# Kernel optimization log

Hardware: AMD Instinct MI355X
Metric: run time of the kernel (lower is better)

Reference implementation:

```python
import jax, jax.numpy as jnp
import numpy as np

THRESHOLD = 0.5
NEG_POS_RATIO = 3
ALPHA = 1.0
BETA = 1.0
IGNORE_INDEX = 255

B, P, C, O = 16, 16384, 21, 16
H = W = 256


def cxcy_to_xy(c):
    return jnp.concatenate([c[..., :2] - c[..., 2:] / 2, c[..., :2] + c[..., 2:] / 2], axis=-1)


def xy_to_cxcy(xy):
    return jnp.concatenate([(xy[..., :2] + xy[..., 2:]) / 2, xy[..., 2:] - xy[..., :2]], axis=-1)


def cxcy_to_gcxgcy(cxcy, priors_cxcy):
    return jnp.concatenate([
        (cxcy[..., :2] - priors_cxcy[..., :2]) / (priors_cxcy[..., 2:] / 10.0),
        jnp.log(cxcy[..., 2:] / priors_cxcy[..., 2:]) * 5.0,
    ], axis=-1)


def jaccard(set1, set2):
    # set1 [O,4] xy, set2 [P,4] xy -> IoU [O,P]
    lo = jnp.maximum(set1[:, None, :2], set2[None, :, :2])
    hi = jnp.minimum(set1[:, None, 2:], set2[None, :, 2:])
    wh = jnp.clip(hi - lo, 0.0)
    inter = wh[..., 0] * wh[..., 1]
    a1 = (set1[:, 2] - set1[:, 0]) * (set1[:, 3] - set1[:, 1])
    a2 = (set2[:, 2] - set2[:, 0]) * (set2[:, 3] - set2[:, 1])
    return inter / (a1[:, None] + a2[None, :] - inter)


def setup_inputs() -> dict:
    key = jax.random.key(0)
    ks = jax.random.split(key, 8)
    predicted_locs = jax.random.normal(ks[0], (B, P, 4), dtype=jnp.float32)
    predicted_scores = jax.random.normal(ks[1], (B, P, C), dtype=jnp.float32)
    predicted_masks = jax.random.normal(ks[2], (B, C, H, W), dtype=jnp.float32)
    x1y1 = jax.random.uniform(ks[3], (B, O, 2), dtype=jnp.float32) * 0.8
    wh = jax.random.uniform(ks[4], (B, O, 2), dtype=jnp.float32) * 0.19 + 0.01
    boxes = jnp.concatenate([x1y1, x1y1 + wh], axis=-1)  # valid xy boxes
    pc = jax.random.uniform(ks[5], (P, 2), dtype=jnp.float32) * 0.9 + 0.05
    pwh = jax.random.uniform(ks[6], (P, 2), dtype=jnp.float32) * 0.28 + 0.02
    priors_cxcy = jnp.concatenate([pc, pwh], axis=-1)
    labels = jax.random.randint(ks[7], (B, O), 1, C)  # object labels, never background
    masks = jax.random.randint(jax.random.fold_in(key, 99), (B, 1, H, W), 0, C)
    return {
        'predicted_locs': predicted_locs,
        'predicted_scores': predicted_scores,
        'predicted_masks': predicted_masks,
        'boxes': boxes,
        'priors_cxcy': priors_cxcy,
        'labels': labels,
        'masks': masks,
    }


def _assign(bx, lb, priors_cxcy, priors_xy):
    # bx [O,4] xy, lb [O] int -> true_locs [P,4], true_classes [P]
    ov = jaccard(bx, priors_xy)  # [O,P]
    overlap_for_each_prior = ov.max(axis=0)       # [P]
    object_for_each_prior = ov.argmax(axis=0)     # [P]
    prior_for_each_object = ov.argmax(axis=1)     # [O]
    # guarantee every object is matched to its best prior
    object_for_each_prior = object_for_each_prior.at[prior_for_each_object].set(jnp.arange(O))
    overlap_for_each_prior = overlap_for_each_prior.at[prior_for_each_object].set(1.0)
    label_for_each_prior = lb[object_for_each_prior]
    label_for_each_prior = jnp.where(overlap_for_each_prior < THRESHOLD, 0, label_for_each_prior)
    true_locs = cxcy_to_gcxgcy(xy_to_cxcy(bx[object_for_each_prior]), priors_cxcy)
    return true_locs, label_for_each_prior


def reference(predicted_locs, predicted_scores, predicted_masks, boxes, priors_cxcy, labels, masks):
    priors_xy = cxcy_to_xy(priors_cxcy)
    true_locs, true_classes = jax.vmap(_assign, in_axes=(0, 0, None, None))(
        boxes, labels, priors_cxcy, priors_xy)  # [B,P,4], [B,P]

    pos = true_classes != 0                      # [B,P]
    pos_f = pos.astype(predicted_locs.dtype)
    n_pos = pos.sum(axis=1)                      # [B]

    # localization: L1Loss (mean over positive prior elements)
    diff = jnp.abs(predicted_locs - true_locs)
    loc_loss = (diff * pos_f[..., None]).sum() / jnp.maximum(pos_f.sum() * 4.0, 1.0)

    # confidence: CE per prior + hard negative mining
    logp = jax.nn.log_softmax(predicted_scores, axis=-1)            # [B,P,C]
    ce = -jnp.take_along_axis(logp, true_classes[..., None], axis=-1)[..., 0]  # [B,P]
    ce_pos_sum = (ce * pos_f).sum()
    ce_neg = jnp.where(pos, 0.0, ce)
    ce_neg_sorted = -jnp.sort(-ce_neg, axis=1)                      # descending
    ranks = jnp.arange(P)[None, :]
    hard = (ranks < (NEG_POS_RATIO * n_pos)[:, None]).astype(ce.dtype)
    ce_hardneg_sum = (ce_neg_sorted * hard).sum()
    conf_loss = (ce_hardneg_sum + ce_pos_sum) / n_pos.sum().astype(ce.dtype)

    # mask loss: cross_entropy2d, sum reduction then / (H*W) / B
    tgt = masks[:, 0]                                                # [B,H,W]
    valid = (tgt != IGNORE_INDEX)
    t = jnp.where(valid, tgt, 0)
    logp_m = jax.nn.log_softmax(predicted_masks, axis=1)             # [B,C,H,W]
    ce_m = -jnp.take_along_axis(logp_m, t[:, None], axis=1)[:, 0]    # [B,H,W]
    mask_loss = (ce_m * valid.astype(ce_m.dtype)).sum() / (H * W) / B

    return conf_loss + ALPHA * loc_loss + BETA * mask_loss
```

## Files before the change

kernel.cpp:

```cpp
#include <hip/hip_runtime.h>
#include <cstdint>
#include <cstddef>

#define Bn 16
#define Pn 16384
#define Cn 21
#define On 16
#define HWn 65536
#define THRESH 0.5f

typedef float f4v __attribute__((ext_vector_type(4)));


__device__ __forceinline__ float waveReduceSum(float v) {
  for (int off = 32; off > 0; off >>= 1) v += __shfl_down(v, off, 64);
  return v;
}
__device__ __forceinline__ int waveReduceSumI(int v) {
  for (int off = 32; off > 0; off >>= 1) v += __shfl_down(v, off, 64);
  return v;
}

__global__ __launch_bounds__(256) void k_phase1(
    const float* __restrict__ boxes, const float* __restrict__ priors,
    unsigned long long* __restrict__ partials, int* __restrict__ done_cnt) {
  const int lane = threadIdx.x & 63, wave = threadIdx.x >> 6;
  __shared__ float4 sbox[On];
  __shared__ float sarea[On];
  __shared__ unsigned long long skey[On];
  if (blockIdx.x == 0 && threadIdx.x == 0) *done_cnt = 0;

  const int b = blockIdx.x >> 6;
  const int p0 = (blockIdx.x & 63) << 8;
  const int p = p0 + threadIdx.x;
  if (threadIdx.x < On) {
    float4 bx = ((const float4*)boxes)[b * On + threadIdx.x];
    sbox[threadIdx.x] = bx;
    sarea[threadIdx.x] = (bx.z - bx.x) * (bx.w - bx.y);
    skey[threadIdx.x] = 0ULL;
  }
  __syncthreads();
  float4 pr = ((const float4*)priors)[p];
  const float px1 = pr.x - 0.5f * pr.z, py1 = pr.y - 0.5f * pr.w;
  const float px2 = pr.x + 0.5f * pr.z, py2 = pr.y + 0.5f * pr.w;
  const float parea = pr.z * pr.w;
#pragma unroll
  for (int o = 0; o < On; ++o) {
    float4 bx = sbox[o];
    float ix = fmaxf(fminf(px2, bx.z) - fmaxf(px1, bx.x), 0.f);
    float iy = fmaxf(fminf(py2, bx.w) - fmaxf(py1, bx.y), 0.f);
    float inter = ix * iy;
    float iou = inter / (sarea[o] + parea - inter);
    float m = iou;
#pragma unroll
    for (int off = 32; off > 0; off >>= 1) m = fmaxf(m, __shfl_xor(m, off, 64));
    unsigned long long tie = __ballot(iou == m);
    if (lane == 0) {
      int lmin = __ffsll(tie) - 1;
      unsigned minp = (unsigned)(p0 + (wave << 6) + lmin);
      unsigned long long key = ((unsigned long long)__float_as_uint(m) << 32) |
                               (unsigned long long)(0xFFFFFFFFu - minp);
      atomicMax(&skey[o], key);
    }
  }
  __syncthreads();
  if (threadIdx.x < On)
    partials[(size_t)blockIdx.x * On + threadIdx.x] = skey[threadIdx.x];
}

__global__ __launch_bounds__(256, 2) void k_assign(
    const float* __restrict__ plocs, const float* __restrict__ pscores,
    const float* __restrict__ boxes, const float* __restrict__ priors,
    const int* __restrict__ labels, const unsigned long long* __restrict__ partials,
    float* __restrict__ ce_neg, float* __restrict__ apart_loc,
    float* __restrict__ apart_ce, int* __restrict__ apart_npos) {
  __shared__ float ssc[256 * Cn];
  __shared__ float4 sbox[On];
  __shared__ float sarea[On];
  __shared__ int slab[On];
  __shared__ int spfo[On];
  __shared__ unsigned long long skey[On];
  __shared__ float sr1[4], sr2[4];
  __shared__ int sri[4];
  const int lane = threadIdx.x & 63, wave = threadIdx.x >> 6;
  const int b = blockIdx.x >> 6;
  const int p0 = (blockIdx.x & 63) << 8;
  const int p = p0 + threadIdx.x;
  {
    const float4* src = (const float4*)(pscores + ((size_t)b * Pn + p0) * Cn);
    float4* dst = (float4*)ssc;
#pragma unroll
    for (int i = threadIdx.x; i < (256 * Cn) / 4; i += 256) dst[i] = src[i];
  }
  if (threadIdx.x < On) {
    float4 bx = ((const float4*)boxes)[b * On + threadIdx.x];
    sbox[threadIdx.x] = bx;
    sarea[threadIdx.x] = (bx.z - bx.x) * (bx.w - bx.y);
    slab[threadIdx.x] = labels[b * On + threadIdx.x];
    skey[threadIdx.x] = 0ULL;
  }
  __syncthreads();
  {
    const int o = threadIdx.x & 15, j = threadIdx.x >> 4;
    const unsigned long long* pp = partials + ((size_t)b * 64) * On;
    unsigned long long k = 0ULL;
#pragma unroll
    for (int t = 0; t < 4; ++t) {
      unsigned long long v = pp[(size_t)(j * 4 + t) * On + o];
      k = v > k ? v : k;
    }
    atomicMax(&skey[o], k);
  }
  __syncthreads();
  if (threadIdx.x < On)
    spfo[threadIdx.x] = (int)(0xFFFFFFFFu - (unsigned)(skey[threadIdx.x] & 0xFFFFFFFFULL));
  __syncthreads();

  float4 pr = ((const float4*)priors)[p];
  const float px1 = pr.x - 0.5f * pr.z, py1 = pr.y - 0.5f * pr.w;
  const float px2 = pr.x + 0.5f * pr.z, py2 = pr.y + 0.5f * pr.w;
  const float parea = pr.z * pr.w;
  float best = -1.f;
  int bobj = 0;
#pragma unroll
  for (int o = 0; o < On; ++o) {
    float4 bx = sbox[o];
    float ix = fmaxf(fminf(px2, bx.z) - fmaxf(px1, bx.x), 0.f);
    float iy = fmaxf(fminf(py2, bx.w) - fmaxf(py1, bx.y), 0.f);
    float inter = ix * iy;
    float iou = inter / (sarea[o] + parea - inter);
    if (iou > best) { best = iou; bobj = o; }
  }
#pragma unroll
  for (int o = 0; o < On; ++o) {
    if (spfo[o] == p) { bobj = o; best = 1.0f; }
  }
  const int lbl = (best < THRESH) ? 0 : slab[bobj];
  const bool pos = (lbl != 0);
  float locp = 0.f;
  if (pos) {
    float4 bx = sbox[bobj];
    float cx = 0.5f * (bx.x + bx.z), cy = 0.5f * (bx.y + bx.w);
    float w = bx.z - bx.x, h = bx.w - bx.y;
    float g0 = (cx - pr.x) / (pr.z * 0.1f);
    float g1 = (cy - pr.y) / (pr.w * 0.1f);
    float g2 = logf(w / pr.z) * 5.f;
    float g3 = logf(h / pr.w) * 5.f;
    float4 pl = ((const float4*)plocs)[b * Pn + p];
    locp = fabsf(pl.x - g0) + fabsf(pl.y - g1) + fabsf(pl.z - g2) + fabsf(pl.w - g3);
  }
  const float* my = ssc + threadIdx.x * Cn;
  float s = 0.f, xt = 0.f;
#pragma unroll
  for (int c = 0; c < Cn; ++c) {
    float v = my[c];
    s += __expf(v);
    if (c == lbl) xt = v;
  }
  float ce = __logf(s) - xt;
  ce_neg[b * Pn + p] = pos ? 0.f : ce;
  float cep = pos ? ce : 0.f;

  float r1 = waveReduceSum(locp);
  float r2 = waveReduceSum(cep);
  int ri = waveReduceSumI(pos ? 1 : 0);
  if (lane == 0) { sr1[wave] = r1; sr2[wave] = r2; sri[wave] = ri; }
  __syncthreads();
  if (threadIdx.x == 0) {
    apart_loc[blockIdx.x] = sr1[0] + sr1[1] + sr1[2] + sr1[3];
    apart_ce[blockIdx.x] = sr2[0] + sr2[1] + sr2[2] + sr2[3];
    apart_npos[blockIdx.x] = sri[0] + sri[1] + sri[2] + sri[3];
  }
}

__global__ __launch_bounds__(512, 4) void k_hnmask_final(
    const float* __restrict__ ce_neg, const int* __restrict__ apart_npos,
    const float* __restrict__ apart_loc, const float* __restrict__ apart_ce,
    const float* __restrict__ pm, const int* __restrict__ msk,
    float* __restrict__ bres, float* __restrict__ mpart,
    int* __restrict__ done_cnt, float* __restrict__ out) {
  const int tid = threadIdx.x;
  const int lane = tid & 63, wave = tid >> 6;
  __shared__ int scnt[8];
  __shared__ float ssum[8];
  __shared__ float sce[8], smk[8], shn[8];
  __shared__ int sK;
  __shared__ int stick;

  if (blockIdx.x < Bn) {
    const int b = blockIdx.x;
    unsigned rv[32];
#pragma unroll
    for (int i = 0; i < 32; ++i)
      rv[i] = __float_as_uint(ce_neg[b * Pn + i * 512 + tid]);
    if (wave == 0) {
      int v = apart_npos[b * 64 + lane];
      v = waveReduceSumI(v);
      if (lane == 0) sK = v;
    }
    __syncthreads();
    int K = 3 * sK;
    if (K > Pn) K = Pn;
    unsigned lo = 0u, hi = 0x7F800000u;
    while (lo < hi) {
      unsigned mid = lo + ((hi - lo) >> 1);
      int c = 0;
#pragma unroll
      for (int i = 0; i < 32; ++i) c += (rv[i] > mid) ? 1 : 0;
      c = waveReduceSumI(c);
      if (lane == 0) scnt[wave] = c;
      __syncthreads();
      int total = 0;
#pragma unroll
      for (int w = 0; w < 8; ++w) total += scnt[w];
      if (total < K) hi = mid; else lo = mid + 1;
      __syncthreads();
    }
    const float fv = __uint_as_float(lo);
    float s = 0.f;
    int c = 0;
#pragma unroll
    for (int i = 0; i < 32; ++i) {
      if (rv[i] > lo) { s += __uint_as_float(rv[i]); c++; }
    }
    s = waveReduceSum(s);
    c = waveReduceSumI(c);
    if (lane == 0) { ssum[wave] = s; scnt[wave] = c; }
    __syncthreads();
    if (tid == 0) {
      float tots = 0.f;
      int totc = 0;
#pragma unroll
      for (int w = 0; w < 8; ++w) { tots += ssum[w]; totc += scnt[w]; }
      bres[b] = tots + (float)(K - totc) * fv;
    }
  } else {
    const int t = blockIdx.x - Bn;
    float contrib = 0.f;
#pragma unroll
    for (int q = 0; q < 2; ++q) {
      const int idx4 = t * 1024 + q * 512 + tid;
      const int b = idx4 >> 14;
      const int pix = (idx4 & 16383) << 2;
      int4 t4 = ((const int4*)msk)[idx4];
      const float* base = pm + (size_t)b * ((size_t)Cn * HWn) + pix;
#define M_LD(i)                                                              \
  f4v v##i;                                                                  \
  {                                                                          \
    const float* a##i = base + (size_t)(i) * HWn;                            \
    asm volatile("global_load_dwordx4 %0, %1, off"                           \
                 : "=&v"(v##i) : "v"(a##i));                                 \
  }
      M_LD(0) M_LD(1) M_LD(2) M_LD(3) M_LD(4) M_LD(5) M_LD(6) M_LD(7)
      M_LD(8) M_LD(9) M_LD(10) M_LD(11) M_LD(12) M_LD(13) M_LD(14) M_LD(15)
      M_LD(16) M_LD(17) M_LD(18) M_LD(19) M_LD(20)
#undef M_LD
      asm volatile("s_waitcnt vmcnt(0)" ::: "memory");
      __builtin_amdgcn_sched_barrier(0);
      const bool w0 = (t4.x != 255), w1 = (t4.y != 255), w2 = (t4.z != 255),
                 w3 = (t4.w != 255);
      const int c0 = w0 ? t4.x : 0, c1 = w1 ? t4.y : 0, c2 = w2 ? t4.z : 0,
                c3 = w3 ? t4.w : 0;
      float s0 = 0.f, s1 = 0.f, s2 = 0.f, s3 = 0.f;
      float x0 = 0.f, x1 = 0.f, x2 = 0.f, x3 = 0.f;
#define M_ACC(i)                                                             \
  {                                                                          \
    s0 += __expf(v##i.x); s1 += __expf(v##i.y);                              \
    s2 += __expf(v##i.z); s3 += __expf(v##i.w);                              \
    if (c0 == i) x0 = v##i.x; if (c1 == i) x1 = v##i.y;                      \
    if (c2 == i) x2 = v##i.z; if (c3 == i) x3 = v##i.w;                      \
  }
      M_ACC(0) M_ACC(1) M_ACC(2) M_ACC(3) M_ACC(4) M_ACC(5) M_ACC(6) M_ACC(7)
      M_ACC(8) M_ACC(9) M_ACC(10) M_ACC(11) M_ACC(12) M_ACC(13) M_ACC(14)
      M_ACC(15) M_ACC(16) M_ACC(17) M_ACC(18) M_ACC(19) M_ACC(20)
#undef M_ACC
      contrib += (w0 ? (__logf(s0) - x0) : 0.f) +
                 (w1 ? (__logf(s1) - x1) : 0.f) +
                 (w2 ? (__logf(s2) - x2) : 0.f) +
                 (w3 ? (__logf(s3) - x3) : 0.f);
    }
    float r = waveReduceSum(contrib);
    if (lane == 0) ssum[wave] = r;
    __syncthreads();
    if (tid == 0) {
      float acc = 0.f;
#pragma unroll
      for (int w = 0; w < 8; ++w) acc += ssum[w];
      mpart[t] = acc;
    }
  }

  __syncthreads();
  if (tid == 0) {
    __threadfence();
    stick = atomicAdd(done_cnt, 1);
  }
  __syncthreads();
  if (stick != Bn + 256 - 1) return;
  __threadfence();
  float l_loc = apart_loc[tid] + apart_loc[tid + 512];
  float l_ce = apart_ce[tid] + apart_ce[tid + 512];
  int l_np = apart_npos[tid] + apart_npos[tid + 512];
  float l_msk = (tid < 256) ? atomicAdd(&mpart[tid], 0.f) : 0.f;
  float l_hn = (tid < Bn) ? atomicAdd(&bres[tid], 0.f) : 0.f;
  l_loc = waveReduceSum(l_loc);
  l_ce = waveReduceSum(l_ce);
  l_msk = waveReduceSum(l_msk);
  l_hn = waveReduceSum(l_hn);
  int l_npw = waveReduceSumI(l_np);
  if (lane == 0) {
    ssum[wave] = l_loc;
    sce[wave] = l_ce;
    smk[wave] = l_msk;
    shn[wave] = l_hn;
    scnt[wave] = l_npw;
  }
  __syncthreads();
  if (tid == 0) {
    float a0 = 0.f, a1 = 0.f, a2 = 0.f, a3 = 0.f;
    int np_i = 0;
#pragma unroll
    for (int w = 0; w < 8; ++w) {
      a0 += ssum[w]; a1 += sce[w]; a3 += smk[w]; a2 += shn[w];
      np_i += scnt[w];
    }
    float np = (float)np_i;
    float conf = (a2 + a1) / np;
    float loc = a0 / fmaxf(np * 4.f, 1.f);
    float maskl = a3 / (float)HWn / (float)Bn;
    out[0] = conf + loc + maskl;
  }
}

extern "C" void kernel_launch(void* const* d_in, const int* in_sizes, int n_in,
                              void* d_out, int out_size, void* d_ws, size_t ws_size,
                              hipStream_t stream) {
  const float* plocs   = (const float*)d_in[0];
  const float* pscores = (const float*)d_in[1];
  const float* pmasks  = (const float*)d_in[2];
  const float* boxes   = (const float*)d_in[3];
  const float* priors  = (const float*)d_in[4];
  const int*   labels  = (const int*)d_in[5];
  const int*   masks   = (const int*)d_in[6];

  char* ws = (char*)d_ws;
  float* mpart = (float*)ws;
  unsigned long long* partials = (unsigned long long*)(ws + 4096);
  float* ce_neg = (float*)(ws + 135168);
  float* apart_loc = (float*)(ws + 1183744);
  float* apart_ce = (float*)(ws + 1187840);
  int* apart_npos = (int*)(ws + 1191936);
  float* bres = (float*)(ws + 1196032);
  int* done_cnt = (int*)(ws + 1196160);

  k_phase1<<<1024, 256, 0, stream>>>(boxes, priors, partials, done_cnt);
  k_assign<<<1024, 256, 0, stream>>>(plocs, pscores, boxes, priors, labels,
                                     partials, ce_neg, apart_loc, apart_ce,
                                     apart_npos);
  k_hnmask_final<<<Bn + 256, 512, 0, stream>>>(ce_neg, apart_npos, apart_loc,
                                               apart_ce, pmasks, masks, bres,
                                               mpart, done_cnt, (float*)d_out);
}
```

Measured before the change: 190.2 us.

## Spread mask cross-entropy slices across all three kernels to overlap with assignment

The 256 mask-loss slices, which all ran in the final kernel, are now split: 86 run alongside phase-1 IoU matching, 85 alongside assignment/CE, and 85 alongside hard-negative mining. Phase-1 and assign blocks are widened to 512 threads, each handling two prior tiles. The aim is to fill the GPU with memory-bound mask work while the lighter stages run, and to shorten the tail of the last kernel. In exchange the block roles become heterogeneous, and assign blocks need twice the shared memory, which may cut occupancy.

```diff
diff --git a/kernel.cpp b/kernel.cpp
--- a/kernel.cpp
+++ b/kernel.cpp
@@ -21,26 +21,95 @@
   return v;
 }
 
-__global__ __launch_bounds__(256) void k_phase1(
+__device__ __forceinline__ void maskSlice(const float* __restrict__ pm,
+                                          const int* __restrict__ msk,
+                                          float* __restrict__ mpart,
+                                          int m, int tid, float* ssum8) {
+  const int lane = tid & 63, wv = tid >> 6;
+  float contrib = 0.f;
+#pragma unroll
+  for (int q = 0; q < 2; ++q) {
+    const int idx4 = m * 1024 + q * 512 + tid;
+    const int b = idx4 >> 14;
+    const int pix = (idx4 & 16383) << 2;
+    int4 t4 = ((const int4*)msk)[idx4];
+    const float* base = pm + (size_t)b * ((size_t)Cn * HWn) + pix;
+#define M_LD(i)                                                              \
+  f4v v##i;                                                                  \
+  {                                                                          \
+    const float* a##i = base + (size_t)(i) * HWn;                            \
+    asm volatile("global_load_dwordx4 %0, %1, off"                           \
+                 : "=&v"(v##i) : "v"(a##i));                                 \
+  }
+    M_LD(0) M_LD(1) M_LD(2) M_LD(3) M_LD(4) M_LD(5) M_LD(6) M_LD(7)
+    M_LD(8) M_LD(9) M_LD(10) M_LD(11) M_LD(12) M_LD(13) M_LD(14) M_LD(15)
+    M_LD(16) M_LD(17) M_LD(18) M_LD(19) M_LD(20)
+#undef M_LD
+    asm volatile("s_waitcnt vmcnt(0)" ::: "memory");
+    __builtin_amdgcn_sched_barrier(0);
+    const bool w0 = (t4.x != 255), w1 = (t4.y != 255), w2 = (t4.z != 255),
+               w3 = (t4.w != 255);
+    const int c0 = w0 ? t4.x : 0, c1 = w1 ? t4.y : 0, c2 = w2 ? t4.z : 0,
+              c3 = w3 ? t4.w : 0;
+    float s0 = 0.f, s1 = 0.f, s2 = 0.f, s3 = 0.f;
+    float x0 = 0.f, x1 = 0.f, x2 = 0.f, x3 = 0.f;
+#define M_ACC(i)                                                             \
+  {                                                                          \
+    s0 += __expf(v##i.x); s1 += __expf(v##i.y);                              \
+    s2 += __expf(v##i.z); s3 += __expf(v##i.w);                              \
+    if (c0 == i) x0 = v##i.x; if (c1 == i) x1 = v##i.y;                      \
+    if (c2 == i) x2 = v##i.z; if (c3 == i) x3 = v##i.w;                      \
+  }
+    M_ACC(0) M_ACC(1) M_ACC(2) M_ACC(3) M_ACC(4) M_ACC(5) M_ACC(6) M_ACC(7)
+    M_ACC(8) M_ACC(9) M_ACC(10) M_ACC(11) M_ACC(12) M_ACC(13) M_ACC(14)
+    M_ACC(15) M_ACC(16) M_ACC(17) M_ACC(18) M_ACC(19) M_ACC(20)
+#undef M_ACC
+    contrib += (w0 ? (__logf(s0) - x0) : 0.f) +
+               (w1 ? (__logf(s1) - x1) : 0.f) +
+               (w2 ? (__logf(s2) - x2) : 0.f) +
+               (w3 ? (__logf(s3) - x3) : 0.f);
+  }
+  float r = waveReduceSum(contrib);
+  if (lane == 0) ssum8[wv] = r;
+  __syncthreads();
+  if (tid == 0) {
+    float acc = 0.f;
+#pragma unroll
+    for (int w = 0; w < 8; ++w) acc += ssum8[w];
+    mpart[m] = acc;
+  }
+}
+
+__global__ __launch_bounds__(512, 4) void k1_p1mask(
     const float* __restrict__ boxes, const float* __restrict__ priors,
-    unsigned long long* __restrict__ partials, int* __restrict__ done_cnt) {
-  const int lane = threadIdx.x & 63, wave = threadIdx.x >> 6;
+    const float* __restrict__ pm, const int* __restrict__ msk,
+    unsigned long long* __restrict__ partials, float* __restrict__ mpart,
+    int* __restrict__ done_cnt) {
   __shared__ float4 sbox[On];
   __shared__ float sarea[On];
-  __shared__ unsigned long long skey[On];
-  if (blockIdx.x == 0 && threadIdx.x == 0) *done_cnt = 0;
-
-  const int b = blockIdx.x >> 6;
-  const int p0 = (blockIdx.x & 63) << 8;
-  const int p = p0 + threadIdx.x;
-  if (threadIdx.x < On) {
-    float4 bx = ((const float4*)boxes)[b * On + threadIdx.x];
-    sbox[threadIdx.x] = bx;
-    sarea[threadIdx.x] = (bx.z - bx.x) * (bx.w - bx.y);
-    skey[threadIdx.x] = 0ULL;
-  }
-  __syncthreads();
-  float4 pr = ((const float4*)priors)[p];
+  __shared__ unsigned long long skey2[2][On];
+  __shared__ float ssum8[8];
+  const int tid = threadIdx.x;
+  if (blockIdx.x == 0 && tid == 0) *done_cnt = 0;
+
+  if (blockIdx.x < 86) {
+    maskSlice(pm, msk, mpart, blockIdx.x, tid, ssum8);
+    return;
+  }
+  const int T = blockIdx.x - 86;
+  const int h = tid >> 8, t256 = tid & 255;
+  const int lane = tid & 63;
+  const int task = 2 * T + h;
+  const int b = task >> 6;
+  const int p0 = (task & 63) << 8;
+  if (tid < On) {
+    float4 bx = ((const float4*)boxes)[b * On + tid];
+    sbox[tid] = bx;
+    sarea[tid] = (bx.z - bx.x) * (bx.w - bx.y);
+  }
+  if (t256 < On) skey2[h][t256] = 0ULL;
+  __syncthreads();
+  float4 pr = ((const float4*)priors)[p0 + t256];
   const float px1 = pr.x - 0.5f * pr.z, py1 = pr.y - 0.5f * pr.w;
   const float px2 = pr.x + 0.5f * pr.z, py2 = pr.y + 0.5f * pr.w;
   const float parea = pr.z * pr.w;
@@ -57,51 +126,61 @@
     unsigned long long tie = __ballot(iou == m);
     if (lane == 0) {
       int lmin = __ffsll(tie) - 1;
-      unsigned minp = (unsigned)(p0 + (wave << 6) + lmin);
+      unsigned minp = (unsigned)(p0 + ((t256 >> 6) << 6) + lmin);
       unsigned long long key = ((unsigned long long)__float_as_uint(m) << 32) |
                                (unsigned long long)(0xFFFFFFFFu - minp);
-      atomicMax(&skey[o], key);
-    }
-  }
-  __syncthreads();
-  if (threadIdx.x < On)
-    partials[(size_t)blockIdx.x * On + threadIdx.x] = skey[threadIdx.x];
-}
-
-__global__ __launch_bounds__(256, 2) void k_assign(
+      atomicMax(&skey2[h][o], key);
+    }
+  }
+  __syncthreads();
+  if (t256 < On)
+    partials[(size_t)task * On + t256] = skey2[h][t256];
+}
+
+__global__ __launch_bounds__(512, 4) void k2_assignmask(
     const float* __restrict__ plocs, const float* __restrict__ pscores,
     const float* __restrict__ boxes, const float* __restrict__ priors,
     const int* __restrict__ labels, const unsigned long long* __restrict__ partials,
+    const float* __restrict__ pm, const int* __restrict__ msk,
     float* __restrict__ ce_neg, float* __restrict__ apart_loc,
-    float* __restrict__ apart_ce, int* __restrict__ apart_npos) {
-  __shared__ float ssc[256 * Cn];
+    float* __restrict__ apart_ce, int* __restrict__ apart_npos,
+    float* __restrict__ mpart) {
+  __shared__ float ssc[2 * 256 * Cn];
   __shared__ float4 sbox[On];
   __shared__ float sarea[On];
   __shared__ int slab[On];
   __shared__ int spfo[On];
   __shared__ unsigned long long skey[On];
-  __shared__ float sr1[4], sr2[4];
-  __shared__ int sri[4];
-  const int lane = threadIdx.x & 63, wave = threadIdx.x >> 6;
-  const int b = blockIdx.x >> 6;
-  const int p0 = (blockIdx.x & 63) << 8;
-  const int p = p0 + threadIdx.x;
+  __shared__ float sr1[8], sr2[8];
+  __shared__ int sri[8];
+  const int tid = threadIdx.x;
+  if (blockIdx.x < 85) {
+    maskSlice(pm, msk, mpart, 86 + blockIdx.x, tid, sr1);
+    return;
+  }
+  const int T = blockIdx.x - 85;
+  const int h = tid >> 8, t256 = tid & 255;
+  const int lane = tid & 63, wv = tid >> 6;
+  const int task = 2 * T + h;
+  const int b = task >> 6;
+  const int p0 = (task & 63) << 8;
+  const int p = p0 + t256;
   {
     const float4* src = (const float4*)(pscores + ((size_t)b * Pn + p0) * Cn);
-    float4* dst = (float4*)ssc;
-#pragma unroll
-    for (int i = threadIdx.x; i < (256 * Cn) / 4; i += 256) dst[i] = src[i];
-  }
-  if (threadIdx.x < On) {
-    float4 bx = ((const float4*)boxes)[b * On + threadIdx.x];
-    sbox[threadIdx.x] = bx;
-    sarea[threadIdx.x] = (bx.z - bx.x) * (bx.w - bx.y);
-    slab[threadIdx.x] = labels[b * On + threadIdx.x];
-    skey[threadIdx.x] = 0ULL;
-  }
-  __syncthreads();
-  {
-    const int o = threadIdx.x & 15, j = threadIdx.x >> 4;
+    float4* dst = (float4*)(ssc + h * (256 * Cn));
+#pragma unroll
+    for (int i = t256; i < (256 * Cn) / 4; i += 256) dst[i] = src[i];
+  }
+  if (tid < On) {
+    float4 bx = ((const float4*)boxes)[b * On + tid];
+    sbox[tid] = bx;
+    sarea[tid] = (bx.z - bx.x) * (bx.w - bx.y);
+    slab[tid] = labels[b * On + tid];
+    skey[tid] = 0ULL;
+  }
+  __syncthreads();
+  if (tid < 256) {
+    const int o = tid & 15, j = tid >> 4;
     const unsigned long long* pp = partials + ((size_t)b * 64) * On;
     unsigned long long k = 0ULL;
 #pragma unroll
@@ -112,8 +191,8 @@
     atomicMax(&skey[o], k);
   }
   __syncthreads();
-  if (threadIdx.x < On)
-    spfo[threadIdx.x] = (int)(0xFFFFFFFFu - (unsigned)(skey[threadIdx.x] & 0xFFFFFFFFULL));
+  if (tid < On)
+    spfo[tid] = (int)(0xFFFFFFFFu - (unsigned)(skey[tid] & 0xFFFFFFFFULL));
   __syncthreads();
 
   float4 pr = ((const float4*)priors)[p];
@@ -141,15 +220,16 @@
   if (pos) {
     float4 bx = sbox[bobj];
     float cx = 0.5f * (bx.x + bx.z), cy = 0.5f * (bx.y + bx.w);
-    float w = bx.z - bx.x, h = bx.w - bx.y;
+    float w = bx.z - bx.x, hh = bx.w - bx.y;
     float g0 = (cx - pr.x) / (pr.z * 0.1f);
     float g1 = (cy - pr.y) / (pr.w * 0.1f);
     float g2 = logf(w / pr.z) * 5.f;
-    float g3 = logf(h / pr.w) * 5.f;
+    float g3 = logf(hh / pr.w) * 5.f;
     float4 pl = ((const float4*)plocs)[b * Pn + p];
-    locp = fabsf(pl.x - g0) + fabsf(pl.y - g1) + fabsf(pl.z - g2) + fabsf(pl.w - g3);
-  }
-  const float* my = ssc + threadIdx.x * Cn;
+    locp = fabsf(pl.x - g0) + fabsf(pl.y - g1) + fabsf(pl.z - g2) +
+           fabsf(pl.w - g3);
+  }
+  const float* my = ssc + h * (256 * Cn) + t256 * Cn;
   float s = 0.f, xt = 0.f;
 #pragma unroll
   for (int c = 0; c < Cn; ++c) {
@@ -164,23 +244,28 @@
   float r1 = waveReduceSum(locp);
   float r2 = waveReduceSum(cep);
   int ri = waveReduceSumI(pos ? 1 : 0);
-  if (lane == 0) { sr1[wave] = r1; sr2[wave] = r2; sri[wave] = ri; }
-  __syncthreads();
-  if (threadIdx.x == 0) {
-    apart_loc[blockIdx.x] = sr1[0] + sr1[1] + sr1[2] + sr1[3];
-    apart_ce[blockIdx.x] = sr2[0] + sr2[1] + sr2[2] + sr2[3];
-    apart_npos[blockIdx.x] = sri[0] + sri[1] + sri[2] + sri[3];
-  }
-}
-
-__global__ __launch_bounds__(512, 4) void k_hnmask_final(
+  if (lane == 0) { sr1[wv] = r1; sr2[wv] = r2; sri[wv] = ri; }
+  __syncthreads();
+  if (tid == 0) {
+    apart_loc[task] = sr1[0] + sr1[1] + sr1[2] + sr1[3];
+    apart_ce[task] = sr2[0] + sr2[1] + sr2[2] + sr2[3];
+    apart_npos[task] = sri[0] + sri[1] + sri[2] + sri[3];
+  }
+  if (tid == 256) {
+    apart_loc[task] = sr1[4] + sr1[5] + sr1[6] + sr1[7];
+    apart_ce[task] = sr2[4] + sr2[5] + sr2[6] + sr2[7];
+    apart_npos[task] = sri[4] + sri[5] + sri[6] + sri[7];
+  }
+}
+
+__global__ __launch_bounds__(512, 4) void k3_hnmask_final(
     const float* __restrict__ ce_neg, const int* __restrict__ apart_npos,
     const float* __restrict__ apart_loc, const float* __restrict__ apart_ce,
     const float* __restrict__ pm, const int* __restrict__ msk,
     float* __restrict__ bres, float* __restrict__ mpart,
     int* __restrict__ done_cnt, float* __restrict__ out) {
   const int tid = threadIdx.x;
-  const int lane = tid & 63, wave = tid >> 6;
+  const int lane = tid & 63, wv = tid >> 6;
   __shared__ int scnt[8];
   __shared__ float ssum[8];
   __shared__ float sce[8], smk[8], shn[8];
@@ -193,7 +278,7 @@
 #pragma unroll
     for (int i = 0; i < 32; ++i)
       rv[i] = __float_as_uint(ce_neg[b * Pn + i * 512 + tid]);
-    if (wave == 0) {
+    if (wv == 0) {
       int v = apart_npos[b * 64 + lane];
       v = waveReduceSumI(v);
       if (lane == 0) sK = v;
@@ -208,7 +293,7 @@
 #pragma unroll
       for (int i = 0; i < 32; ++i) c += (rv[i] > mid) ? 1 : 0;
       c = waveReduceSumI(c);
-      if (lane == 0) scnt[wave] = c;
+      if (lane == 0) scnt[wv] = c;
       __syncthreads();
       int total = 0;
 #pragma unroll
@@ -225,7 +310,7 @@
     }
     s = waveReduceSum(s);
     c = waveReduceSumI(c);
-    if (lane == 0) { ssum[wave] = s; scnt[wave] = c; }
+    if (lane == 0) { ssum[wv] = s; scnt[wv] = c; }
     __syncthreads();
     if (tid == 0) {
       float tots = 0.f;
@@ -235,59 +320,7 @@
       bres[b] = tots + (float)(K - totc) * fv;
     }
   } else {
-    const int t = blockIdx.x - Bn;
-    float contrib = 0.f;
-#pragma unroll
-    for (int q = 0; q < 2; ++q) {
-      const int idx4 = t * 1024 + q * 512 + tid;
-      const int b = idx4 >> 14;
-      const int pix = (idx4 & 16383) << 2;
-      int4 t4 = ((const int4*)msk)[idx4];
-      const float* base = pm + (size_t)b * ((size_t)Cn * HWn) + pix;
-#define M_LD(i)                                                              \
-  f4v v##i;                                                                  \
-  {                                                                          \
-    const float* a##i = base + (size_t)(i) * HWn;                            \
-    asm volatile("global_load_dwordx4 %0, %1, off"                           \
-                 : "=&v"(v##i) : "v"(a##i));                                 \
-  }
-      M_LD(0) M_LD(1) M_LD(2) M_LD(3) M_LD(4) M_LD(5) M_LD(6) M_LD(7)
-      M_LD(8) M_LD(9) M_LD(10) M_LD(11) M_LD(12) M_LD(13) M_LD(14) M_LD(15)
-      M_LD(16) M_LD(17) M_LD(18) M_LD(19) M_LD(20)
-#undef M_LD
-      asm volatile("s_waitcnt vmcnt(0)" ::: "memory");
-      __builtin_amdgcn_sched_barrier(0);
-      const bool w0 = (t4.x != 255), w1 = (t4.y != 255), w2 = (t4.z != 255),
-                 w3 = (t4.w != 255);
-      const int c0 = w0 ? t4.x : 0, c1 = w1 ? t4.y : 0, c2 = w2 ? t4.z : 0,
-                c3 = w3 ? t4.w : 0;
-      float s0 = 0.f, s1 = 0.f, s2 = 0.f, s3 = 0.f;
-      float x0 = 0.f, x1 = 0.f, x2 = 0.f, x3 = 0.f;
-#define M_ACC(i)                                                             \
-  {                                                                          \
-    s0 += __expf(v##i.x); s1 += __expf(v##i.y);                              \
-    s2 += __expf(v##i.z); s3 += __expf(v##i.w);                              \
-    if (c0 == i) x0 = v##i.x; if (c1 == i) x1 = v##i.y;                      \
-    if (c2 == i) x2 = v##i.z; if (c3 == i) x3 = v##i.w;                      \
-  }
-      M_ACC(0) M_ACC(1) M_ACC(2) M_ACC(3) M_ACC(4) M_ACC(5) M_ACC(6) M_ACC(7)
-      M_ACC(8) M_ACC(9) M_ACC(10) M_ACC(11) M_ACC(12) M_ACC(13) M_ACC(14)
-      M_ACC(15) M_ACC(16) M_ACC(17) M_ACC(18) M_ACC(19) M_ACC(20)
-#undef M_ACC
-      contrib += (w0 ? (__logf(s0) - x0) : 0.f) +
-                 (w1 ? (__logf(s1) - x1) : 0.f) +
-                 (w2 ? (__logf(s2) - x2) : 0.f) +
-                 (w3 ? (__logf(s3) - x3) : 0.f);
-    }
-    float r = waveReduceSum(contrib);
-    if (lane == 0) ssum[wave] = r;
-    __syncthreads();
-    if (tid == 0) {
-      float acc = 0.f;
-#pragma unroll
-      for (int w = 0; w < 8; ++w) acc += ssum[w];
-      mpart[t] = acc;
-    }
+    maskSlice(pm, msk, mpart, 171 + (blockIdx.x - Bn), tid, ssum);
   }
 
   __syncthreads();
@@ -296,7 +329,7 @@
     stick = atomicAdd(done_cnt, 1);
   }
   __syncthreads();
-  if (stick != Bn + 256 - 1) return;
+  if (stick != Bn + 85 - 1) return;
   __threadfence();
   float l_loc = apart_loc[tid] + apart_loc[tid + 512];
   float l_ce = apart_ce[tid] + apart_ce[tid + 512];
@@ -309,11 +342,11 @@
   l_hn = waveReduceSum(l_hn);
   int l_npw = waveReduceSumI(l_np);
   if (lane == 0) {
-    ssum[wave] = l_loc;
-    sce[wave] = l_ce;
-    smk[wave] = l_msk;
-    shn[wave] = l_hn;
-    scnt[wave] = l_npw;
+    ssum[wv] = l_loc;
+    sce[wv] = l_ce;
+    smk[wv] = l_msk;
+    shn[wv] = l_hn;
+    scnt[wv] = l_npw;
   }
   __syncthreads();
   if (tid == 0) {
@@ -353,11 +386,12 @@
   float* bres = (float*)(ws + 1196032);
   int* done_cnt = (int*)(ws + 1196160);
 
-  k_phase1<<<1024, 256, 0, stream>>>(boxes, priors, partials, done_cnt);
-  k_assign<<<1024, 256, 0, stream>>>(plocs, pscores, boxes, priors, labels,
-                                     partials, ce_neg, apart_loc, apart_ce,
-                                     apart_npos);
-  k_hnmask_final<<<Bn + 256, 512, 0, stream>>>(ce_neg, apart_npos, apart_loc,
-                                               apart_ce, pmasks, masks, bres,
-                                               mpart, done_cnt, (float*)d_out);
-}
+  k1_p1mask<<<598, 512, 0, stream>>>(boxes, priors, pmasks, masks, partials,
+                                     mpart, done_cnt);
+  k2_assignmask<<<597, 512, 0, stream>>>(plocs, pscores, boxes, priors, labels,
+                                         partials, pmasks, masks, ce_neg,
+                                         apart_loc, apart_ce, apart_npos, mpart);
+  k3_hnmask_final<<<101, 512, 0, stream>>>(ce_neg, apart_npos, apart_loc,
+                                           apart_ce, pmasks, masks, bres,
+                                           mpart, done_cnt, (float*)d_out);
+}
```

Result: no change. 190.6 us (+0.2%).
